# Kernel optimization log

Hardware: AMD Instinct MI355X
Metric: run time of the kernel (lower is better)

Reference implementation:

```python
import math
import jax, jax.numpy as jnp
import numpy as np

GROUPS = 8
EPS = 1e-5


def setup_inputs() -> dict:
    key = jax.random.key(0)
    ks = jax.random.split(key, 4)
    B, C, H, W = 4, 128, 64, 64
    x = jax.random.normal(ks[0], (B, C, H, W), dtype=jnp.float32)
    norm_w = jnp.ones((C,), dtype=jnp.float32)
    norm_b = jnp.zeros((C,), dtype=jnp.float32)
    qkv_w = jax.random.normal(ks[1], (3 * C, C), dtype=jnp.float32) * 0.02
    qkv_b = jnp.zeros((3 * C,), dtype=jnp.float32)
    proj_w = jax.random.normal(ks[2], (C, C), dtype=jnp.float32) * 0.02
    proj_b = jnp.zeros((C,), dtype=jnp.float32)
    return {"x": x, "norm_w": norm_w, "norm_b": norm_b,
            "qkv_w": qkv_w, "qkv_b": qkv_b,
            "proj_w": proj_w, "proj_b": proj_b}


def reference(x, norm_w, norm_b, qkv_w, qkv_b, proj_w, proj_b):
    B, C, H, W = x.shape
    N = H * W
    # GroupNorm over (C/G, H, W) per group
    xr = x.reshape(B, GROUPS, C // GROUPS, N)
    mean = xr.mean(axis=(2, 3), keepdims=True)
    var = xr.var(axis=(2, 3), keepdims=True)
    h = ((xr - mean) * jax.lax.rsqrt(var + EPS)).reshape(B, C, N)
    h = h * norm_w[None, :, None] + norm_b[None, :, None]
    # 1x1 conv QKV == per-pixel linear: [B, 3C, N]
    qkv = jnp.einsum('oc,bcn->bon', qkv_w, h) + qkv_b[None, :, None]
    q, k, v = jnp.split(qkv, 3, axis=1)  # each [B, C, N]
    scale = 1.0 / math.sqrt(C)
    attn = jax.nn.softmax(jnp.einsum('bci,bcj->bij', q, k) * scale, axis=-1)  # [B,N,N]
    out = jnp.einsum('bij,bcj->bci', attn, v)  # [B, C, N]
    proj = jnp.einsum('oc,bcn->bon', proj_w, out) + proj_b[None, :, None]
    return x + proj.reshape(B, C, H, W)
```

## Files before the change

### kernel.cpp

```cpp
#include <hip/hip_runtime.h>

typedef float  f32x4  __attribute__((ext_vector_type(4)));
typedef short  bf16x8 __attribute__((ext_vector_type(8)));
typedef unsigned short u16;

constexpr int B_ = 4;
constexpr int C_ = 128;
constexpr int N_ = 4096;
constexpr int G_ = 8;
constexpr int CperG = 16;
constexpr float EPS_ = 1e-5f;
constexpr float SCALE_ = 0.08838834764831845f;

__device__ inline u16 f2bf(float f) {
    union { float f; unsigned u; } v; v.f = f;
    unsigned r = v.u + 0x7fffu + ((v.u >> 16) & 1u);
    return (u16)(r >> 16);
}
__device__ inline unsigned pk2(float a, float b) {
    return (unsigned)f2bf(a) | ((unsigned)f2bf(b) << 16);
}
__device__ inline void gload16(const u16* g, u16* l) {
    __builtin_amdgcn_global_load_lds(
        (const __attribute__((address_space(1))) void*)g,
        (__attribute__((address_space(3))) void*)l, 16, 0, 0);
}

__global__ __launch_bounds__(256) void prep_kernel(const float* __restrict__ x,
                                                   const float* __restrict__ qw,
                                                   const float* __restrict__ pw,
                                                   float* __restrict__ stats2,
                                                   u16* __restrict__ qwbf,
                                                   u16* __restrict__ pwbf) {
    int blk = blockIdx.x;
    if (blk < 256) {
        __shared__ float rs[4], rss[4];
        int bg = blk >> 3, chunk = blk & 7;
        const float4* xp = (const float4*)(x + (size_t)bg * (CperG * N_)) + chunk * 2048;
        float s = 0.f, ss = 0.f;
        for (int i = threadIdx.x; i < 2048; i += 256) {
            float4 v = xp[i];
            s  += v.x + v.y + v.z + v.w;
            ss += v.x*v.x + v.y*v.y + v.z*v.z + v.w*v.w;
        }
        #pragma unroll
        for (int off = 32; off > 0; off >>= 1) {
            s  += __shfl_down(s, off);
            ss += __shfl_down(ss, off);
        }
        int wv = threadIdx.x >> 6, ln = threadIdx.x & 63;
        if (ln == 0) { rs[wv] = s; rss[wv] = ss; }
        __syncthreads();
        if (threadIdx.x == 0) {
            stats2[blk*2]     = rs[0] + rs[1] + rs[2] + rs[3];
            stats2[blk*2 + 1] = rss[0] + rss[1] + rss[2] + rss[3];
        }
    } else {
        int fidx = ((blk - 256) * 256 + threadIdx.x) * 4;
        float4 v;
        u16* dst;
        if (fidx < 3*C_*C_) { v = *(const float4*)(qw + fidx); dst = qwbf + fidx; }
        else { int j = fidx - 3*C_*C_; v = *(const float4*)(pw + j); dst = pwbf + j; }
        ushort4 o;
        o.x = f2bf(v.x); o.y = f2bf(v.y); o.z = f2bf(v.z); o.w = f2bf(v.w);
        *(ushort4*)dst = o;
    }
}

constexpr int HS = 136;

__global__ __launch_bounds__(256, 2) void qkv_kernel(const float* __restrict__ x,
                                                     const float* __restrict__ stats2,
                                                     const float* __restrict__ nw,
                                                     const float* __restrict__ nb,
                                                     const u16* __restrict__ qwbf,
                                                     const float* __restrict__ qb,
                                                     u16* __restrict__ Qt,
                                                     u16* __restrict__ Kt,
                                                     u16* __restrict__ Vb,
                                                     float* __restrict__ qn2,
                                                     int* __restrict__ kmaxI) {
    int n0 = (blockIdx.x & 63) * 64;
    int b  = blockIdx.x >> 6;
    __shared__ u16 hs[64 * HS];
    __shared__ u16 Wl[64 * HS];
    __shared__ float gmean[8], grstd[8];
    int t = threadIdx.x;
    const float invM = 1.f / (float)(CperG * N_);
    if (t < 8) {
        const float* sp = stats2 + (size_t)(b*G_ + t)*16;
        float S = 0.f, SS = 0.f;
        #pragma unroll
        for (int k2 = 0; k2 < 8; ++k2) { S += sp[k2*2]; SS += sp[k2*2 + 1]; }
        float mean = S * invM;
        gmean[t] = mean;
        grstd[t] = rsqrtf(SS * invM - mean*mean + EPS_);
    }
    __syncthreads();
    #pragma unroll
    for (int r = 0; r < 8; ++r) {
        int idx = t + (r << 8);
        int c = idx >> 4, n4 = idx & 15;
        int g = c >> 4;
        float wgt = nw[c] * grstd[g];
        float bia = nb[c] - gmean[g] * wgt;
        float4 xv = *(const float4*)(x + ((size_t)(b*C_ + c))*N_ + n0 + n4*4);
        int base = (n4*4) * HS + c;
        hs[base         ] = f2bf(xv.x*wgt + bia);
        hs[base +     HS] = f2bf(xv.y*wgt + bia);
        hs[base + 2 * HS] = f2bf(xv.z*wgt + bia);
        hs[base + 3 * HS] = f2bf(xv.w*wgt + bia);
    }
    __syncthreads();
    int w = t >> 6, lane = t & 63, lo = lane & 15, hi = lane >> 4;
    bf16x8 hf[4];
    #pragma unroll
    for (int ch = 0; ch < 4; ++ch)
        hf[ch] = *(const bf16x8*)(hs + (16*w + lo)*HS + 32*ch + 8*hi);

    float nq = 0.f, nk = 0.f;
    for (int ck = 0; ck < 6; ++ck) {
        {
            int r = t >> 2, p = t & 3;
            const u16* src = qwbf + (size_t)(ck*64 + r)*C_ + p*32;
            u16* dst = Wl + r*HS + p*32;
            #pragma unroll
            for (int k2 = 0; k2 < 4; ++k2)
                *(uint4*)(dst + 8*k2) = *(const uint4*)(src + 8*k2);
        }
        __syncthreads();
        #pragma unroll
        for (int ot = 0; ot < 4; ++ot) {
            int o16 = ck*64 + ot*16;
            bf16x8 wf[4];
            #pragma unroll
            for (int ch = 0; ch < 4; ++ch)
                wf[ch] = *(const bf16x8*)(Wl + (ot*16 + lo)*HS + 32*ch + 8*hi);
            if (o16 < 2*C_) {
                f32x4 acc = (f32x4){0.f, 0.f, 0.f, 0.f};
                #pragma unroll
                for (int ch = 0; ch < 4; ++ch)
                    acc = __builtin_amdgcn_mfma_f32_16x16x32_bf16(wf[ch], hf[ch], acc, 0, 0, 0);
                float4 bv = *(const float4*)(qb + o16 + 4*hi);
                int n = n0 + 16*w + lo;
                ushort4 o4;
                if (o16 < C_) {
                    float q0 = (acc[0] + bv.x) * SCALE_;
                    float q1 = (acc[1] + bv.y) * SCALE_;
                    float q2 = (acc[2] + bv.z) * SCALE_;
                    float q3 = (acc[3] + bv.w) * SCALE_;
                    nq += (q0*q0 + q1*q1) + (q2*q2 + q3*q3);
                    o4.x = f2bf(q0); o4.y = f2bf(q1); o4.z = f2bf(q2); o4.w = f2bf(q3);
                    *(ushort4*)(Qt + ((size_t)b*N_ + n)*C_ + o16 + 4*hi) = o4;
                } else {
                    float k0 = acc[0] + bv.x, k1 = acc[1] + bv.y;
                    float k2 = acc[2] + bv.z, k3 = acc[3] + bv.w;
                    nk += (k0*k0 + k1*k1) + (k2*k2 + k3*k3);
                    o4.x = f2bf(k0); o4.y = f2bf(k1); o4.z = f2bf(k2); o4.w = f2bf(k3);
                    *(ushort4*)(Kt + ((size_t)b*N_ + n)*C_ + (o16 - C_) + 4*hi) = o4;
                }
            } else {
                f32x4 acc = (f32x4){0.f, 0.f, 0.f, 0.f};
                #pragma unroll
                for (int ch = 0; ch < 4; ++ch)
                    acc = __builtin_amdgcn_mfma_f32_16x16x32_bf16(hf[ch], wf[ch], acc, 0, 0, 0);
                float bia = qb[o16 + lo];
                ushort4 o4;
                o4.x = f2bf(acc[0] + bia);
                o4.y = f2bf(acc[1] + bia);
                o4.z = f2bf(acc[2] + bia);
                o4.w = f2bf(acc[3] + bia);
                *(ushort4*)(Vb + ((size_t)b*C_ + (o16 - 2*C_) + lo)*N_ + n0 + 16*w + 4*hi) = o4;
            }
        }
        __syncthreads();
    }
    nq += __shfl_xor(nq, 16); nq += __shfl_xor(nq, 32);
    nk += __shfl_xor(nk, 16); nk += __shfl_xor(nk, 32);
    if (lane < 16) qn2[(size_t)b*N_ + n0 + 16*w + lo] = nq;
    #pragma unroll
    for (int off = 1; off < 16; off <<= 1)
        nk = fmaxf(nk, __shfl_xor(nk, off));
    if (lane == 0) atomicMax(&kmaxI[b], __float_as_int(nk));
}

constexpr int PS = 40;

__global__ __launch_bounds__(256, 2) void attn_kernel(const u16* __restrict__ Qt,
                                                      const u16* __restrict__ Kt,
                                                      const u16* __restrict__ Vb,
                                                      const float* __restrict__ qn2,
                                                      const int* __restrict__ kmaxI,
                                                      const u16* __restrict__ pwbf,
                                                      const float* __restrict__ pb,
                                                      const float* __restrict__ x,
                                                      float* __restrict__ out) {
    int lb = blockIdx.x;
    int b  = lb & 3;
    int i0 = 32 * (lb >> 2);
    int t = threadIdx.x;
    int w = t >> 6, lane = t & 63, lo = lane & 15, hi = lane >> 4;
    int qg = w >> 1, ks = w & 1;

    const u16* Qb = Qt + (size_t)b*N_*C_;
    const u16* Kb = Kt + (size_t)b*N_*C_;
    const u16* Vv = Vb + (size_t)b*C_*N_;

    __shared__ __align__(16) u16 KV[16384];
    __shared__ __align__(16) u16 Ps[4 * 16 * PS];
    __shared__ float lW[4][16];
    u16* Kl = KV;
    u16* Vl = KV + 8192;
    u16* Pw = Ps + w * 16 * PS;
    float* Ob = (float*)KV;

    float kmax = sqrtf(__int_as_float(kmaxI[b]));
    float mq = sqrtf(qn2[(size_t)b*N_ + i0 + 16*qg + lo]) * kmax * 1.02f + 1e-6f;

    bf16x8 qf[4];
    #pragma unroll
    for (int ch = 0; ch < 4; ++ch)
        qf[ch] = *(const bf16x8*)(Qb + (size_t)(i0 + 16*qg + lo)*C_ + 32*ch + 8*hi);

    f32x4 acc[8];
    #pragma unroll
    for (int ct = 0; ct < 8; ++ct) acc[ct] = (f32x4){0.f, 0.f, 0.f, 0.f};
    float psum = 0.f;

    int srow  = lane >> 4;
    int schnk = lane & 15;
    int vrow  = lane >> 3;
    int vchnk = lane & 7;

    for (int it = 0; it < 64; ++it) {
        int tile0 = it * 64;
        if (w < 2) {
            #pragma unroll
            for (int j = 0; j < 8; ++j) {
                int k0 = 32*w + 4*j;
                int r  = k0 + srow;
                const u16* g = Kb + (size_t)(tile0 + r)*C_ + (schnk ^ (r & 15))*8;
                gload16(g, Kl + k0*128);
            }
        } else {
            #pragma unroll
            for (int j = 0; j < 8; ++j) {
                int c0 = 64*(w - 2) + 8*j;
                int ch = c0 + vrow;
                const u16* g = Vv + (size_t)ch*N_ + tile0 + (vchnk ^ (ch & 7))*8;
                gload16(g, Vl + c0*64);
            }
        }
        __syncthreads();
        f32x4 s0 = (f32x4){0.f,0.f,0.f,0.f}, s1 = s0;
        #pragma unroll
        for (int ch = 0; ch < 4; ++ch) {
            int kk0 = 32*ks + lo, kk1 = kk0 + 16;
            bf16x8 k0f = *(const bf16x8*)(Kl + kk0*128 + (((4*ch + hi) ^ lo))*8);
            bf16x8 k1f = *(const bf16x8*)(Kl + kk1*128 + (((4*ch + hi) ^ lo))*8);
            s0 = __builtin_amdgcn_mfma_f32_16x16x32_bf16(k0f, qf[ch], s0, 0, 0, 0);
            s1 = __builtin_amdgcn_mfma_f32_16x16x32_bf16(k1f, qf[ch], s1, 0, 0, 0);
        }
        {
            float p0 = __expf(s0[0]-mq), p1 = __expf(s0[1]-mq);
            float p2 = __expf(s0[2]-mq), p3 = __expf(s0[3]-mq);
            psum += (p0+p1)+(p2+p3);
            uint2 pk; pk.x = pk2(p0,p1); pk.y = pk2(p2,p3);
            *(uint2*)(Pw + lo*PS + 4*hi) = pk;
        }
        {
            float p0 = __expf(s1[0]-mq), p1 = __expf(s1[1]-mq);
            float p2 = __expf(s1[2]-mq), p3 = __expf(s1[3]-mq);
            psum += (p0+p1)+(p2+p3);
            uint2 pk; pk.x = pk2(p0,p1); pk.y = pk2(p2,p3);
            *(uint2*)(Pw + lo*PS + 16 + 4*hi) = pk;
        }
        bf16x8 pa = *(const bf16x8*)(Pw + lo*PS + 8*hi);
        #pragma unroll
        for (int ct = 0; ct < 8; ++ct) {
            int cc = 16*ct + lo;
            bf16x8 vf = *(const bf16x8*)(Vl + cc*64 + (((4*ks + hi) ^ (cc & 7)))*8);
            acc[ct] = __builtin_amdgcn_mfma_f32_16x16x32_bf16(pa, vf, acc[ct], 0, 0, 0);
        }
        __syncthreads();
    }

    psum += __shfl_xor(psum, 16);
    psum += __shfl_xor(psum, 32);
    if (lane < 16) lW[w][lo] = psum;
    for (int i = 0; i < 2; ++i) {
        if (ks == i) {
            #pragma unroll
            for (int ct = 0; ct < 8; ++ct)
                #pragma unroll
                for (int r = 0; r < 4; ++r) {
                    int q = 16*qg + 4*hi + r, c = 16*ct + lo;
                    if (i == 0) Ob[q*132 + c]  = acc[ct][r];
                    else        Ob[q*132 + c] += acc[ct][r];
                }
        }
        __syncthreads();
    }
    float linv = 1.f / (lW[2*qg][lo] + lW[2*qg + 1][lo]);
    bf16x8 aa[4];
    #pragma unroll
    for (int ch = 0; ch < 4; ++ch) {
        float4 ua = *(const float4*)(Ob + (16*qg + lo)*132 + 32*ch + 8*hi);
        float4 ub = *(const float4*)(Ob + (16*qg + lo)*132 + 32*ch + 8*hi + 4);
        union { bf16x8 h; unsigned u[4]; } pkd;
        pkd.u[0] = pk2(ua.x*linv, ua.y*linv);
        pkd.u[1] = pk2(ua.z*linv, ua.w*linv);
        pkd.u[2] = pk2(ub.x*linv, ub.y*linv);
        pkd.u[3] = pk2(ub.z*linv, ub.w*linv);
        aa[ch] = pkd.h;
    }
    #pragma unroll
    for (int ot = 0; ot < 4; ++ot) {
        int ob = 64*ks + 16*ot;
        f32x4 pr = (f32x4){0.f, 0.f, 0.f, 0.f};
        #pragma unroll
        for (int ch = 0; ch < 4; ++ch) {
            bf16x8 bw = *(const bf16x8*)(pwbf + (size_t)(ob + lo)*C_ + 32*ch + 8*hi);
            pr = __builtin_amdgcn_mfma_f32_16x16x32_bf16(aa[ch], bw, pr, 0, 0, 0);
        }
        int o = ob + lo;
        float pbv = pb[o];
        size_t base = ((size_t)(b*C_ + o))*N_ + i0 + 16*qg + 4*hi;
        float4 xr = *(const float4*)(x + base);
        float4 res;
        res.x = xr.x + pr[0] + pbv;
        res.y = xr.y + pr[1] + pbv;
        res.z = xr.z + pr[2] + pbv;
        res.w = xr.w + pr[3] + pbv;
        *(float4*)(out + base) = res;
    }
}

extern "C" void kernel_launch(void* const* d_in, const int* in_sizes, int n_in,
                              void* d_out, int out_size, void* d_ws, size_t ws_size,
                              hipStream_t stream) {
    const float* x  = (const float*)d_in[0];
    const float* nw = (const float*)d_in[1];
    const float* nb = (const float*)d_in[2];
    const float* qw = (const float*)d_in[3];
    const float* qb = (const float*)d_in[4];
    const float* pw = (const float*)d_in[5];
    const float* pb = (const float*)d_in[6];
    float* out = (float*)d_out;

    char* p = (char*)d_ws;
    float* stats2 = (float*)p;                 p += 2048;
    float* qn2    = (float*)p;                 p += (size_t)B_*N_*4;
    int*   kmaxI  = (int*)p;                   p += 256;
    u16*   qwbf   = (u16*)p;                   p += (size_t)3*C_*C_*2;
    u16*   pwbf   = (u16*)p;                   p += (size_t)C_*C_*2;
    u16*   Qt     = (u16*)p;                   p += (size_t)B_*N_*C_*2;
    u16*   Kt     = (u16*)p;                   p += (size_t)B_*N_*C_*2;
    u16*   Vb     = (u16*)p;

    prep_kernel<<<dim3(320), 256, 0, stream>>>(x, qw, pw, stats2, qwbf, pwbf);
    qkv_kernel<<<dim3(256), 256, 0, stream>>>(x, stats2, nw, nb, qwbf, qb,
                                              Qt, Kt, Vb, qn2, kmaxI);
    attn_kernel<<<dim3(512), 256, 0, stream>>>(Qt, Kt, Vb, qn2, kmaxI,
                                               pwbf, pb, x, out);
}
```

Measured before the change: 180.9 us.

## Double-buffer K/V tiles and share them across 64 queries per block

The attention kernel now runs 512 threads per block and covers 64 query rows instead of 32, so each loaded K/V tile serves twice as many queries. K and V tiles are double-buffered in LDS: the next tile is loaded asynchronously while MFMAs run on the current one, leaving one barrier per iteration. This cuts global K/V traffic and hides load latency. In exchange it doubles LDS use per block and halves the grid to 256 blocks, which lowers block-level parallelism.

```diff
diff --git a/kernel.cpp b/kernel.cpp
--- a/kernel.cpp
+++ b/kernel.cpp
@@ -186,7 +186,7 @@
 
 constexpr int PS = 40;
 
-__global__ __launch_bounds__(256, 2) void attn_kernel(const u16* __restrict__ Qt,
+__global__ __launch_bounds__(512, 2) void attn_kernel(const u16* __restrict__ Qt,
                                                       const u16* __restrict__ Kt,
                                                       const u16* __restrict__ Vb,
                                                       const float* __restrict__ qn2,
@@ -197,67 +197,87 @@
                                                       float* __restrict__ out) {
     int lb = blockIdx.x;
     int b  = lb & 3;
-    int i0 = 32 * (lb >> 2);
+    int i0 = 64 * (lb >> 2);
     int t = threadIdx.x;
     int w = t >> 6, lane = t & 63, lo = lane & 15, hi = lane >> 4;
-    int qg = w >> 1, ks = w & 1;
+    int qt = w >> 1, ks = w & 1;
 
     const u16* Qb = Qt + (size_t)b*N_*C_;
     const u16* Kb = Kt + (size_t)b*N_*C_;
     const u16* Vv = Vb + (size_t)b*C_*N_;
 
-    __shared__ __align__(16) u16 KV[16384];
-    __shared__ __align__(16) u16 Ps[4 * 16 * PS];
-    __shared__ float lW[4][16];
-    u16* Kl = KV;
-    u16* Vl = KV + 8192;
-    u16* Pw = Ps + w * 16 * PS;
+    __shared__ __align__(16) u16 KV[2][16384];
+    __shared__ __align__(16) u16 Ps[8][16 * PS];
+    __shared__ float lW[8][16];
     float* Ob = (float*)KV;
 
     float kmax = sqrtf(__int_as_float(kmaxI[b]));
-    float mq = sqrtf(qn2[(size_t)b*N_ + i0 + 16*qg + lo]) * kmax * 1.02f + 1e-6f;
+    float mq = sqrtf(qn2[(size_t)b*N_ + i0 + 16*qt + lo]) * kmax * 1.02f + 1e-6f;
 
     bf16x8 qf[4];
     #pragma unroll
     for (int ch = 0; ch < 4; ++ch)
-        qf[ch] = *(const bf16x8*)(Qb + (size_t)(i0 + 16*qg + lo)*C_ + 32*ch + 8*hi);
+        qf[ch] = *(const bf16x8*)(Qb + (size_t)(i0 + 16*qt + lo)*C_ + 32*ch + 8*hi);
 
     f32x4 acc[8];
     #pragma unroll
     for (int ct = 0; ct < 8; ++ct) acc[ct] = (f32x4){0.f, 0.f, 0.f, 0.f};
     float psum = 0.f;
 
-    int srow  = lane >> 4;
-    int schnk = lane & 15;
-    int vrow  = lane >> 3;
-    int vchnk = lane & 7;
-
-    for (int it = 0; it < 64; ++it) {
-        int tile0 = it * 64;
-        if (w < 2) {
-            #pragma unroll
-            for (int j = 0; j < 8; ++j) {
-                int k0 = 32*w + 4*j;
+    int srow = lane >> 4, schnk = lane & 15;
+    int vrow = lane >> 3, vchnk = lane & 7;
+
+    {
+        u16* Kl = KV[0];
+        u16* Vl = KV[0] + 8192;
+        if (w < 4) {
+            #pragma unroll
+            for (int j = 0; j < 4; ++j) {
+                int k0 = 16*w + 4*j;
                 int r  = k0 + srow;
-                const u16* g = Kb + (size_t)(tile0 + r)*C_ + (schnk ^ (r & 15))*8;
-                gload16(g, Kl + k0*128);
+                gload16(Kb + (size_t)r*C_ + (schnk ^ (r & 15))*8, Kl + k0*128);
             }
         } else {
             #pragma unroll
-            for (int j = 0; j < 8; ++j) {
-                int c0 = 64*(w - 2) + 8*j;
+            for (int j = 0; j < 4; ++j) {
+                int c0 = 32*(w - 4) + 8*j;
                 int ch = c0 + vrow;
-                const u16* g = Vv + (size_t)ch*N_ + tile0 + (vchnk ^ (ch & 7))*8;
-                gload16(g, Vl + c0*64);
+                gload16(Vv + (size_t)ch*N_ + (vchnk ^ (ch & 7))*8, Vl + c0*64);
             }
         }
-        __syncthreads();
+    }
+    __syncthreads();
+
+    for (int it = 0; it < 64; ++it) {
+        int cur = it & 1;
+        if (it < 63) {
+            int tile0 = (it + 1) * 64;
+            u16* Kl = KV[cur ^ 1];
+            u16* Vl = KV[cur ^ 1] + 8192;
+            if (w < 4) {
+                #pragma unroll
+                for (int j = 0; j < 4; ++j) {
+                    int k0 = 16*w + 4*j;
+                    int r  = k0 + srow;
+                    gload16(Kb + (size_t)(tile0 + r)*C_ + (schnk ^ (r & 15))*8, Kl + k0*128);
+                }
+            } else {
+                #pragma unroll
+                for (int j = 0; j < 4; ++j) {
+                    int c0 = 32*(w - 4) + 8*j;
+                    int ch = c0 + vrow;
+                    gload16(Vv + (size_t)ch*N_ + tile0 + (vchnk ^ (ch & 7))*8, Vl + c0*64);
+                }
+            }
+        }
+        u16* Kl = KV[cur];
+        u16* Vl = KV[cur] + 8192;
         f32x4 s0 = (f32x4){0.f,0.f,0.f,0.f}, s1 = s0;
+        int kk0 = 32*ks + lo;
         #pragma unroll
         for (int ch = 0; ch < 4; ++ch) {
-            int kk0 = 32*ks + lo, kk1 = kk0 + 16;
-            bf16x8 k0f = *(const bf16x8*)(Kl + kk0*128 + (((4*ch + hi) ^ lo))*8);
-            bf16x8 k1f = *(const bf16x8*)(Kl + kk1*128 + (((4*ch + hi) ^ lo))*8);
+            bf16x8 k0f = *(const bf16x8*)(Kl + kk0*128        + ((4*ch + hi) ^ lo)*8);
+            bf16x8 k1f = *(const bf16x8*)(Kl + (kk0 + 16)*128 + ((4*ch + hi) ^ lo)*8);
             s0 = __builtin_amdgcn_mfma_f32_16x16x32_bf16(k0f, qf[ch], s0, 0, 0, 0);
             s1 = __builtin_amdgcn_mfma_f32_16x16x32_bf16(k1f, qf[ch], s1, 0, 0, 0);
         }
@@ -266,20 +286,20 @@
             float p2 = __expf(s0[2]-mq), p3 = __expf(s0[3]-mq);
             psum += (p0+p1)+(p2+p3);
             uint2 pk; pk.x = pk2(p0,p1); pk.y = pk2(p2,p3);
-            *(uint2*)(Pw + lo*PS + 4*hi) = pk;
+            *(uint2*)(&Ps[w][lo*PS + 4*hi]) = pk;
         }
         {
             float p0 = __expf(s1[0]-mq), p1 = __expf(s1[1]-mq);
             float p2 = __expf(s1[2]-mq), p3 = __expf(s1[3]-mq);
             psum += (p0+p1)+(p2+p3);
             uint2 pk; pk.x = pk2(p0,p1); pk.y = pk2(p2,p3);
-            *(uint2*)(Pw + lo*PS + 16 + 4*hi) = pk;
-        }
-        bf16x8 pa = *(const bf16x8*)(Pw + lo*PS + 8*hi);
+            *(uint2*)(&Ps[w][lo*PS + 16 + 4*hi]) = pk;
+        }
+        bf16x8 pa = *(const bf16x8*)(&Ps[w][lo*PS + 8*hi]);
         #pragma unroll
         for (int ct = 0; ct < 8; ++ct) {
             int cc = 16*ct + lo;
-            bf16x8 vf = *(const bf16x8*)(Vl + cc*64 + (((4*ks + hi) ^ (cc & 7)))*8);
+            bf16x8 vf = *(const bf16x8*)(Vl + cc*64 + ((4*ks + hi) ^ (cc & 7))*8);
             acc[ct] = __builtin_amdgcn_mfma_f32_16x16x32_bf16(pa, vf, acc[ct], 0, 0, 0);
         }
         __syncthreads();
@@ -288,25 +308,26 @@
     psum += __shfl_xor(psum, 16);
     psum += __shfl_xor(psum, 32);
     if (lane < 16) lW[w][lo] = psum;
+    __syncthreads();
     for (int i = 0; i < 2; ++i) {
         if (ks == i) {
             #pragma unroll
             for (int ct = 0; ct < 8; ++ct)
                 #pragma unroll
                 for (int r = 0; r < 4; ++r) {
-                    int q = 16*qg + 4*hi + r, c = 16*ct + lo;
+                    int q = 16*qt + 4*hi + r, c = 16*ct + lo;
                     if (i == 0) Ob[q*132 + c]  = acc[ct][r];
                     else        Ob[q*132 + c] += acc[ct][r];
                 }
         }
         __syncthreads();
     }
-    float linv = 1.f / (lW[2*qg][lo] + lW[2*qg + 1][lo]);
+    float linv = 1.f / (lW[2*qt][lo] + lW[2*qt + 1][lo]);
     bf16x8 aa[4];
     #pragma unroll
     for (int ch = 0; ch < 4; ++ch) {
-        float4 ua = *(const float4*)(Ob + (16*qg + lo)*132 + 32*ch + 8*hi);
-        float4 ub = *(const float4*)(Ob + (16*qg + lo)*132 + 32*ch + 8*hi + 4);
+        float4 ua = *(const float4*)(Ob + (16*qt + lo)*132 + 32*ch + 8*hi);
+        float4 ub = *(const float4*)(Ob + (16*qt + lo)*132 + 32*ch + 8*hi + 4);
         union { bf16x8 h; unsigned u[4]; } pkd;
         pkd.u[0] = pk2(ua.x*linv, ua.y*linv);
         pkd.u[1] = pk2(ua.z*linv, ua.w*linv);
@@ -325,7 +346,7 @@
         }
         int o = ob + lo;
         float pbv = pb[o];
-        size_t base = ((size_t)(b*C_ + o))*N_ + i0 + 16*qg + 4*hi;
+        size_t base = ((size_t)(b*C_ + o))*N_ + i0 + 16*qt + 4*hi;
         float4 xr = *(const float4*)(x + base);
         float4 res;
         res.x = xr.x + pr[0] + pbv;
@@ -361,6 +382,6 @@
     prep_kernel<<<dim3(320), 256, 0, stream>>>(x, qw, pw, stats2, qwbf, pwbf);
     qkv_kernel<<<dim3(256), 256, 0, stream>>>(x, stats2, nw, nb, qwbf, qb,
                                               Qt, Kt, Vb, qn2, kmaxI);
-    attn_kernel<<<dim3(512), 256, 0, stream>>>(Qt, Kt, Vb, qn2, kmaxI,
+    attn_kernel<<<dim3(256), 512, 0, stream>>>(Qt, Kt, Vb, qn2, kmaxI,
                                                pwbf, pb, x, out);
 }
```

Measured after the change: 183.6 us. About the same (+1.5%).

## Restructure attention to 32x32 MFMA, 64-query blocks, and double-buffered K/V tiles

Applied to the files above, without the earlier changes.

The attention kernel now processes 64 queries per block with 8 waves (512 threads), using 32x32x16 bf16 MFMAs instead of 16x16x32. P stays in registers as the B operand, so the LDS round-trip for P is gone. K/V tiles of 128 keys are double-buffered so the next tile loads while the current one computes. This doubles K/V reuse per load and halves block count, at the cost of 128KB of LDS per block, which likely limits occupancy to one block per CU and leaves only 256 blocks.

```diff
diff --git a/kernel.cpp b/kernel.cpp
--- a/kernel.cpp
+++ b/kernel.cpp
@@ -1,7 +1,8 @@
 #include <hip/hip_runtime.h>
 
-typedef float  f32x4  __attribute__((ext_vector_type(4)));
-typedef short  bf16x8 __attribute__((ext_vector_type(8)));
+typedef float  f32x4   __attribute__((ext_vector_type(4)));
+typedef float  f32x16  __attribute__((ext_vector_type(16)));
+typedef short  bf16x8  __attribute__((ext_vector_type(8)));
 typedef unsigned short u16;
 
 constexpr int B_ = 4;
@@ -184,9 +185,7 @@
     if (lane == 0) atomicMax(&kmaxI[b], __float_as_int(nk));
 }
 
-constexpr int PS = 40;
-
-__global__ __launch_bounds__(256, 2) void attn_kernel(const u16* __restrict__ Qt,
+__global__ __launch_bounds__(512, 2) void attn_kernel(const u16* __restrict__ Qt,
                                                       const u16* __restrict__ Kt,
                                                       const u16* __restrict__ Vb,
                                                       const float* __restrict__ qn2,
@@ -197,126 +196,144 @@
                                                       float* __restrict__ out) {
     int lb = blockIdx.x;
     int b  = lb & 3;
-    int i0 = 32 * (lb >> 2);
+    int i0 = 64 * (lb >> 2);
     int t = threadIdx.x;
-    int w = t >> 6, lane = t & 63, lo = lane & 15, hi = lane >> 4;
-    int qg = w >> 1, ks = w & 1;
+    int w = t >> 6, lane = t & 63;
+    int l31 = lane & 31, l15 = lane & 15, h = lane >> 5;
+    int qt = w >> 2, ks = w & 3;
 
     const u16* Qb = Qt + (size_t)b*N_*C_;
     const u16* Kb = Kt + (size_t)b*N_*C_;
     const u16* Vv = Vb + (size_t)b*C_*N_;
 
-    __shared__ __align__(16) u16 KV[16384];
-    __shared__ __align__(16) u16 Ps[4 * 16 * PS];
-    __shared__ float lW[4][16];
-    u16* Kl = KV;
-    u16* Vl = KV + 8192;
-    u16* Pw = Ps + w * 16 * PS;
+    __shared__ __align__(16) u16 KV[2][32768];
+    __shared__ float lW[8][32];
     float* Ob = (float*)KV;
 
     float kmax = sqrtf(__int_as_float(kmaxI[b]));
-    float mq = sqrtf(qn2[(size_t)b*N_ + i0 + 16*qg + lo]) * kmax * 1.02f + 1e-6f;
-
-    bf16x8 qf[4];
-    #pragma unroll
-    for (int ch = 0; ch < 4; ++ch)
-        qf[ch] = *(const bf16x8*)(Qb + (size_t)(i0 + 16*qg + lo)*C_ + 32*ch + 8*hi);
-
-    f32x4 acc[8];
-    #pragma unroll
-    for (int ct = 0; ct < 8; ++ct) acc[ct] = (f32x4){0.f, 0.f, 0.f, 0.f};
+    float mq = sqrtf(qn2[(size_t)b*N_ + i0 + 32*qt + l31]) * kmax * 1.02f + 1e-6f;
+
+    bf16x8 qf[8];
+    #pragma unroll
+    for (int ch = 0; ch < 8; ++ch)
+        qf[ch] = *(const bf16x8*)(Qb + (size_t)(i0 + 32*qt + l31)*C_ + 16*ch + 8*h);
+
+    f32x16 acc[4];
+    #pragma unroll
+    for (int ct = 0; ct < 4; ++ct)
+        #pragma unroll
+        for (int r = 0; r < 16; ++r) acc[ct][r] = 0.f;
     float psum = 0.f;
 
-    int srow  = lane >> 4;
-    int schnk = lane & 15;
-    int vrow  = lane >> 3;
-    int vchnk = lane & 7;
-
-    for (int it = 0; it < 64; ++it) {
-        int tile0 = it * 64;
-        if (w < 2) {
+    int srow = lane >> 4, schnk = lane & 15;
+
+    auto stage = [&](int tile0, u16* buf) {
+        if (w < 4) {
             #pragma unroll
             for (int j = 0; j < 8; ++j) {
                 int k0 = 32*w + 4*j;
                 int r  = k0 + srow;
-                const u16* g = Kb + (size_t)(tile0 + r)*C_ + (schnk ^ (r & 15))*8;
-                gload16(g, Kl + k0*128);
+                gload16(Kb + (size_t)(tile0 + r)*C_ + (schnk ^ (r & 15))*8, buf + k0*128);
             }
         } else {
             #pragma unroll
             for (int j = 0; j < 8; ++j) {
-                int c0 = 64*(w - 2) + 8*j;
-                int ch = c0 + vrow;
-                const u16* g = Vv + (size_t)ch*N_ + tile0 + (vchnk ^ (ch & 7))*8;
-                gload16(g, Vl + c0*64);
+                int c0 = 32*(w - 4) + 4*j;
+                int ch = c0 + srow;
+                gload16(Vv + (size_t)ch*N_ + tile0 + (schnk ^ (ch & 15))*8,
+                        buf + 16384 + c0*128);
             }
         }
-        __syncthreads();
-        f32x4 s0 = (f32x4){0.f,0.f,0.f,0.f}, s1 = s0;
-        #pragma unroll
-        for (int ch = 0; ch < 4; ++ch) {
-            int kk0 = 32*ks + lo, kk1 = kk0 + 16;
-            bf16x8 k0f = *(const bf16x8*)(Kl + kk0*128 + (((4*ch + hi) ^ lo))*8);
-            bf16x8 k1f = *(const bf16x8*)(Kl + kk1*128 + (((4*ch + hi) ^ lo))*8);
-            s0 = __builtin_amdgcn_mfma_f32_16x16x32_bf16(k0f, qf[ch], s0, 0, 0, 0);
-            s1 = __builtin_amdgcn_mfma_f32_16x16x32_bf16(k1f, qf[ch], s1, 0, 0, 0);
-        }
-        {
-            float p0 = __expf(s0[0]-mq), p1 = __expf(s0[1]-mq);
-            float p2 = __expf(s0[2]-mq), p3 = __expf(s0[3]-mq);
-            psum += (p0+p1)+(p2+p3);
-            uint2 pk; pk.x = pk2(p0,p1); pk.y = pk2(p2,p3);
-            *(uint2*)(Pw + lo*PS + 4*hi) = pk;
-        }
-        {
-            float p0 = __expf(s1[0]-mq), p1 = __expf(s1[1]-mq);
-            float p2 = __expf(s1[2]-mq), p3 = __expf(s1[3]-mq);
-            psum += (p0+p1)+(p2+p3);
-            uint2 pk; pk.x = pk2(p0,p1); pk.y = pk2(p2,p3);
-            *(uint2*)(Pw + lo*PS + 16 + 4*hi) = pk;
-        }
-        bf16x8 pa = *(const bf16x8*)(Pw + lo*PS + 8*hi);
-        #pragma unroll
-        for (int ct = 0; ct < 8; ++ct) {
-            int cc = 16*ct + lo;
-            bf16x8 vf = *(const bf16x8*)(Vl + cc*64 + (((4*ks + hi) ^ (cc & 7)))*8);
-            acc[ct] = __builtin_amdgcn_mfma_f32_16x16x32_bf16(pa, vf, acc[ct], 0, 0, 0);
-        }
-        __syncthreads();
-    }
-
-    psum += __shfl_xor(psum, 16);
+    };
+
+    stage(0, KV[0]);
+    __syncthreads();
+
+    for (int it = 0; it < 32; ++it) {
+        int cur = it & 1;
+        if (it < 31) stage((it + 1) * 128, KV[cur ^ 1]);
+        u16* Kl = KV[cur];
+        u16* Vl = KV[cur] + 16384;
+        f32x16 s;
+        #pragma unroll
+        for (int r = 0; r < 16; ++r) s[r] = 0.f;
+        int krow = (32*ks + l31) * 128;
+        #pragma unroll
+        for (int ch = 0; ch < 8; ++ch) {
+            bf16x8 kf = *(const bf16x8*)(Kl + krow + ((2*ch + h) ^ l15)*8);
+            s = __builtin_amdgcn_mfma_f32_32x32x16_bf16(kf, qf[ch], s, 0, 0, 0);
+        }
+        float p[16];
+        #pragma unroll
+        for (int r = 0; r < 16; ++r) {
+            p[r] = __expf(s[r] - mq);
+            psum += p[r];
+        }
+        union { bf16x8 v; unsigned u[4]; } pf1, pf2;
+        pf1.u[0] = pk2(p[0],  p[1]);  pf1.u[1] = pk2(p[2],  p[3]);
+        pf1.u[2] = pk2(p[4],  p[5]);  pf1.u[3] = pk2(p[6],  p[7]);
+        pf2.u[0] = pk2(p[8],  p[9]);  pf2.u[1] = pk2(p[10], p[11]);
+        pf2.u[2] = pk2(p[12], p[13]); pf2.u[3] = pk2(p[14], p[15]);
+        #pragma unroll
+        for (int ct = 0; ct < 4; ++ct) {
+            int vbase = (32*ct + l31) * 128;
+            union { bf16x8 v; long long q[2]; } v1, v2;
+            v1.q[0] = *(const long long*)(Vl + vbase + (2*((4*ks    ) ^ l15) + h)*4);
+            v1.q[1] = *(const long long*)(Vl + vbase + (2*((4*ks + 1) ^ l15) + h)*4);
+            v2.q[0] = *(const long long*)(Vl + vbase + (2*((4*ks + 2) ^ l15) + h)*4);
+            v2.q[1] = *(const long long*)(Vl + vbase + (2*((4*ks + 3) ^ l15) + h)*4);
+            acc[ct] = __builtin_amdgcn_mfma_f32_32x32x16_bf16(v1.v, pf1.v, acc[ct], 0, 0, 0);
+            acc[ct] = __builtin_amdgcn_mfma_f32_32x32x16_bf16(v2.v, pf2.v, acc[ct], 0, 0, 0);
+        }
+        __syncthreads();
+    }
+
     psum += __shfl_xor(psum, 32);
-    if (lane < 16) lW[w][lo] = psum;
-    for (int i = 0; i < 2; ++i) {
+    if (lane < 32) lW[w][l31] = psum;
+    for (int i = 0; i < 4; ++i) {
         if (ks == i) {
-            #pragma unroll
-            for (int ct = 0; ct < 8; ++ct)
+            int q = 32*qt + l31;
+            #pragma unroll
+            for (int ct = 0; ct < 4; ++ct)
                 #pragma unroll
-                for (int r = 0; r < 4; ++r) {
-                    int q = 16*qg + 4*hi + r, c = 16*ct + lo;
-                    if (i == 0) Ob[q*132 + c]  = acc[ct][r];
-                    else        Ob[q*132 + c] += acc[ct][r];
+                for (int qd = 0; qd < 4; ++qd) {
+                    int c = 32*ct + 8*qd + 4*h;
+                    float4 vv;
+                    vv.x = acc[ct][4*qd + 0];
+                    vv.y = acc[ct][4*qd + 1];
+                    vv.z = acc[ct][4*qd + 2];
+                    vv.w = acc[ct][4*qd + 3];
+                    if (i == 0) {
+                        *(float4*)(Ob + q*132 + c) = vv;
+                    } else {
+                        float4 o = *(const float4*)(Ob + q*132 + c);
+                        o.x += vv.x; o.y += vv.y; o.z += vv.z; o.w += vv.w;
+                        *(float4*)(Ob + q*132 + c) = o;
+                    }
                 }
         }
         __syncthreads();
     }
-    float linv = 1.f / (lW[2*qg][lo] + lW[2*qg + 1][lo]);
+    int lo = lane & 15, hi = lane >> 4;
+    int qtile = w >> 1, os = w & 1;
+    int q = 16*qtile + lo;
+    int qg = 4*(q >> 5), qc = q & 31;
+    float linv = 1.f / (lW[qg][qc] + lW[qg+1][qc] + lW[qg+2][qc] + lW[qg+3][qc]);
     bf16x8 aa[4];
     #pragma unroll
     for (int ch = 0; ch < 4; ++ch) {
-        float4 ua = *(const float4*)(Ob + (16*qg + lo)*132 + 32*ch + 8*hi);
-        float4 ub = *(const float4*)(Ob + (16*qg + lo)*132 + 32*ch + 8*hi + 4);
-        union { bf16x8 h; unsigned u[4]; } pkd;
+        float4 ua = *(const float4*)(Ob + q*132 + 32*ch + 8*hi);
+        float4 ub = *(const float4*)(Ob + q*132 + 32*ch + 8*hi + 4);
+        union { bf16x8 hh; unsigned u[4]; } pkd;
         pkd.u[0] = pk2(ua.x*linv, ua.y*linv);
         pkd.u[1] = pk2(ua.z*linv, ua.w*linv);
         pkd.u[2] = pk2(ub.x*linv, ub.y*linv);
         pkd.u[3] = pk2(ub.z*linv, ub.w*linv);
-        aa[ch] = pkd.h;
+        aa[ch] = pkd.hh;
     }
     #pragma unroll
     for (int ot = 0; ot < 4; ++ot) {
-        int ob = 64*ks + 16*ot;
+        int ob = 64*os + 16*ot;
         f32x4 pr = (f32x4){0.f, 0.f, 0.f, 0.f};
         #pragma unroll
         for (int ch = 0; ch < 4; ++ch) {
@@ -325,7 +342,7 @@
         }
         int o = ob + lo;
         float pbv = pb[o];
-        size_t base = ((size_t)(b*C_ + o))*N_ + i0 + 16*qg + 4*hi;
+        size_t base = ((size_t)(b*C_ + o))*N_ + i0 + 16*qtile + 4*hi;
         float4 xr = *(const float4*)(x + base);
         float4 res;
         res.x = xr.x + pr[0] + pbv;
@@ -361,6 +378,6 @@
     prep_kernel<<<dim3(320), 256, 0, stream>>>(x, qw, pw, stats2, qwbf, pwbf);
     qkv_kernel<<<dim3(256), 256, 0, stream>>>(x, stats2, nw, nb, qwbf, qb,
                                               Qt, Kt, Vb, qn2, kmaxI);
-    attn_kernel<<<dim3(512), 256, 0, stream>>>(Qt, Kt, Vb, qn2, kmaxI,
+    attn_kernel<<<dim3(256), 512, 0, stream>>>(Qt, Kt, Vb, qn2, kmaxI,
                                                pwbf, pb, x, out);
 }
```

Result: faster. 169.5 us (-6.3%).
